# Optimization experiments

Measured on AMD Instinct MI355X. Metric: run time of the kernel, lower is better.

Reference implementation:

```python
import jax, jax.numpy as jnp
import numpy as np

N = 100000
E = 1600000
IN_CH = 128
HID = 32
HEADS = 8
OUT_CH = 40
NEG_SLOPE = 0.2


def _glorot(key, shape):
    fan = shape[0] + shape[-1]
    return jax.random.normal(key, shape, dtype=jnp.float32) * jnp.sqrt(2.0 / fan)


def gat_conv(x, src, dst, W, att_src, att_dst, bias, heads, out_ch, concat):
    # PyG GATConv (eval mode, dropout inactive, self-loops already appended)
    n = x.shape[0]
    h = (x @ W).reshape(n, heads, out_ch)              # [N,H,C]
    a_s = jnp.sum(h * att_src, axis=-1)                # [N,H]
    a_d = jnp.sum(h * att_dst, axis=-1)                # [N,H]
    e = jax.nn.leaky_relu(a_s[src] + a_d[dst], NEG_SLOPE)  # [E,H]
    # softmax over incoming edges of each destination node
    m = jax.ops.segment_max(e, dst, num_segments=n)
    e = jnp.exp(e - m[dst])
    denom = jax.ops.segment_sum(e, dst, num_segments=n)
    alpha = e / denom[dst]                              # [E,H]
    msg = h[src] * alpha[:, :, None]                    # [E,H,C] gather + weight
    out = jax.ops.segment_sum(msg, dst, num_segments=n)  # [N,H,C] scatter-add
    if concat:
        out = out.reshape(n, heads * out_ch)
    else:
        out = out.mean(axis=1)
    return out + bias


def setup_inputs() -> dict:
    key = jax.random.key(0)
    ks = jax.random.split(key, 16)
    x = jax.random.normal(ks[0], (N, IN_CH), dtype=jnp.float32)
    edge_index = jax.random.randint(ks[1], (2, E), 0, N, dtype=jnp.int64)
    params = {
        "W1": _glorot(ks[2], (IN_CH, HEADS * HID)),
        "as1": _glorot(ks[3], (HEADS, HID)),
        "ad1": _glorot(ks[4], (HEADS, HID)),
        "b1": jnp.zeros((HEADS * HID,), jnp.float32),
        "W2": _glorot(ks[5], (HEADS * HID, HID)),
        "as2": _glorot(ks[6], (1, HID)),
        "ad2": _glorot(ks[7], (1, HID)),
        "b2": jnp.zeros((HID,), jnp.float32),
        "W3": _glorot(ks[8], (HID, OUT_CH)),
        "as3": _glorot(ks[9], (1, OUT_CH)),
        "ad3": _glorot(ks[10], (1, OUT_CH)),
        "b3": jnp.zeros((OUT_CH,), jnp.float32),
    }
    return {"x": x, "edge_index": edge_index, **params}


def reference(x, edge_index, W1, as1, ad1, b1, W2, as2, ad2, b2, W3, as3, ad3, b3):
    n = x.shape[0]
    # PyG GATConv adds self-loops by default
    loops = jnp.arange(n, dtype=edge_index.dtype)
    src = jnp.concatenate([edge_index[0], loops])
    dst = jnp.concatenate([edge_index[1], loops])

    h = gat_conv(x, src, dst, W1, as1, ad1, b1, HEADS, HID, concat=True)
    h = jax.nn.elu(h)
    h = gat_conv(h, src, dst, W2, as2, ad2, b2, 1, HID, concat=False)
    h = jax.nn.elu(h)
    h = gat_conv(h, src, dst, W3, as3, ad3, b3, 1, OUT_CH, concat=False)
    return jax.nn.log_softmax(h, axis=1)
```

## Files before the change

kernel.cpp:

```cpp
#include <hip/hip_runtime.h>

#define NN 100000
#define NE 1600000
#define ET 1700000
#define NEG 0.2f
#define FNEG 3.4e38f
#define NBSC 98
#define GEMM1_NB 1563
#define PE_NB 6641
#define FATA_NB 8305

#define SRC_OFF   0ULL
#define DST_OFF   6800000ULL
#define RP_OFF    13600000ULL
#define CNT_OFF   14000128ULL
#define CSR_OFF   14400128ULL
#define W1F_OFF   21200128ULL
#define W2F_OFF   21265664ULL
#define W3F_OFF   21282048ULL
#define SC_OFF    21285120ULL
#define H_OFF     21286144ULL
#define H2B_OFF   72486144ULL
#define H3B_OFF   88486144ULL
#define ALPH_OFF  123686144ULL
#define ASN_OFF   150886144ULL
#define ADN_OFF   154086144ULL
#define AS2_OFF   157286144ULL
#define AD2_OFF   157686144ULL
#define WS_NEED   158086144ULL

typedef short bf16x8 __attribute__((ext_vector_type(8)));
typedef float f32x4 __attribute__((ext_vector_type(4)));

__device__ __forceinline__ float lrelu(float x) { return x > 0.f ? x : NEG * x; }
__device__ __forceinline__ float b2f(unsigned short u) {
  return __uint_as_float(((unsigned)u) << 16);
}
__device__ __forceinline__ unsigned short f2bu(float f) {
  unsigned u = __float_as_uint(f);
  return (unsigned short)((u + 0x7FFFu + ((u >> 16) & 1u)) >> 16);
}

__global__ __launch_bounds__(256) void k_sentinel(float* out, int n) {
  int i = blockIdx.x * 256 + threadIdx.x;
  if (i < n) out[i] = 12345.0f;
}

__global__ __launch_bounds__(256) void k_prep_w(const float* __restrict__ W1,
                                                const float* __restrict__ W2,
                                                const float* __restrict__ W3,
                                                unsigned short* __restrict__ W1f,
                                                unsigned short* __restrict__ W2f,
                                                unsigned short* __restrict__ W3f) {
  int idx = blockIdx.x * 256 + threadIdx.x;
  if (idx < 4096) {
    int fg = idx >> 6, lane = idx & 63;
    int mf = fg >> 2, kk = fg & 3;
    int c = mf * 16 + (lane & 15), k0 = kk * 32 + (lane >> 4) * 8;
    unsigned short* o = W1f + idx * 8;
    #pragma unroll
    for (int j = 0; j < 8; ++j) o[j] = f2bu(W1[(k0 + j) * 256 + c]);
  } else if (idx < 5120) {
    int t = idx - 4096;
    int fg = t >> 6, lane = t & 63;
    int mf = fg >> 3, kk = fg & 7;
    int c = mf * 16 + (lane & 15), k0 = kk * 32 + (lane >> 4) * 8;
    unsigned short* o = W2f + t * 8;
    #pragma unroll
    for (int j = 0; j < 8; ++j) o[j] = f2bu(W2[(k0 + j) * 32 + c]);
  } else if (idx < 5312) {
    int t = idx - 5120;
    int mf = t >> 6, lane = t & 63;
    int c = mf * 16 + (lane & 15), k0 = (lane >> 4) * 8;
    unsigned short* o = W3f + t * 8;
    #pragma unroll
    for (int j = 0; j < 8; ++j) o[j] = (c < 40) ? f2bu(W3[(k0 + j) * 40 + c]) : 0;
  }
}

__global__ __launch_bounds__(256) void k_fatA(const int* __restrict__ raw,
                                              int* __restrict__ src,
                                              int* __restrict__ dst,
                                              int* __restrict__ deg,
                                              const float* __restrict__ x,
                                              const bf16x8* __restrict__ W1f,
                                              const float* __restrict__ as1,
                                              const float* __restrict__ ad1,
                                              unsigned short* __restrict__ h,
                                              float* __restrict__ a_s,
                                              float* __restrict__ a_d) {
  __shared__ __align__(16) unsigned short xs[64 * 128];
  __shared__ float asL[256], adL[256];
  const int bid = blockIdx.x;
  const int grp = bid / 5, rem = bid - grp * 5;
  const int tid = threadIdx.x;

  if (rem != 4) {
    int pe = grp * 4 + rem;
    if (pe >= PE_NB) return;
    bool is64 = true;
    #pragma unroll
    for (int i = 1; i < 32; i += 2) is64 = is64 && (raw[i] == 0);
    long long e = (long long)pe * 256 + tid;
    if (e >= ET) return;
    int s, d;
    if (e < NE) {
      if (is64) {
        const long long* r = (const long long*)raw;
        s = (int)r[e];
        d = (int)r[NE + e];
      } else {
        s = raw[e];
        d = raw[NE + e];
      }
    } else {
      s = d = (int)(e - NE);
    }
    src[e] = s;
    dst[e] = d;
    atomicAdd(&deg[d], 1);
    return;
  }

  if (grp >= GEMM1_NB) return;
  const int n0 = grp * 64;
  asL[tid] = as1[tid];
  adL[tid] = ad1[tid];
  for (int j = tid; j < 2048; j += 256) {
    int r = j >> 5;
    int c4 = (j & 31) << 2;
    long long row = n0 + r; if (row >= NN) row = NN - 1;
    float4 v = *(const float4*)(x + row * 128 + c4);
    unsigned short* p = &xs[r * 128 + c4];
    p[0] = f2bu(v.x); p[1] = f2bu(v.y); p[2] = f2bu(v.z); p[3] = f2bu(v.w);
  }
  __syncthreads();
  const int w = tid >> 6, lane = tid & 63;
  const int nloc = w * 16 + (lane & 15);
  const int node = n0 + nloc;
  bf16x8 bfr[4];
  #pragma unroll
  for (int kk = 0; kk < 4; ++kk)
    bfr[kk] = *(const bf16x8*)&xs[nloc * 128 + kk * 32 + (lane >> 4) * 8];
  const int ch_base = (lane >> 4) * 4;
  float sA[8] = {}, sD[8] = {};
  #pragma unroll
  for (int mf = 0; mf < 16; ++mf) {
    f32x4 acc = {0.f, 0.f, 0.f, 0.f};
    #pragma unroll
    for (int kk = 0; kk < 4; ++kk) {
      bf16x8 af = W1f[(mf * 4 + kk) * 64 + lane];
      acc = __builtin_amdgcn_mfma_f32_16x16x32_bf16(af, bfr[kk], acc, 0, 0, 0);
    }
    const float* av = &asL[mf * 16 + ch_base];
    const float* dv = &adL[mf * 16 + ch_base];
    float ps = acc[0] * av[0] + acc[1] * av[1] + acc[2] * av[2] + acc[3] * av[3];
    float pd = acc[0] * dv[0] + acc[1] * dv[1] + acc[2] * dv[2] + acc[3] * dv[3];
    ps += __shfl_xor(ps, 16); ps += __shfl_xor(ps, 32);
    pd += __shfl_xor(pd, 16); pd += __shfl_xor(pd, 32);
    sA[mf >> 1] += ps; sD[mf >> 1] += pd;
    if (node < NN) {
      ushort4 o;
      o.x = f2bu(acc[0]); o.y = f2bu(acc[1]); o.z = f2bu(acc[2]); o.w = f2bu(acc[3]);
      *(ushort4*)&h[(unsigned)(node * 256 + mf * 16 + ch_base)] = o;
    }
  }
  if (lane < 16 && node < NN) {
    #pragma unroll
    for (int hd = 0; hd < 8; ++hd) {
      a_s[node * 8 + hd] = sA[hd];
      a_d[node * 8 + hd] = sD[hd];
    }
  }
}

__global__ __launch_bounds__(1024) void k_scan_a(const int* __restrict__ deg,
                                                 int* __restrict__ rowptr,
                                                 int* __restrict__ bsum) {
  __shared__ int wsum[16];
  const int lane = threadIdx.x & 63, wid = threadIdx.x >> 6;
  int i = blockIdx.x * 1024 + threadIdx.x;
  int x = (i < NN) ? deg[i] : 0;
  int inc = x;
  #pragma unroll
  for (int off = 1; off < 64; off <<= 1) {
    int t = __shfl_up(inc, off);
    if (lane >= off) inc += t;
  }
  if (lane == 63) wsum[wid] = inc;
  __syncthreads();
  if (wid == 0) {
    int w = (lane < 16) ? wsum[lane] : 0;
    #pragma unroll
    for (int off = 1; off < 16; off <<= 1) {
      int t = __shfl_up(w, off);
      if (lane >= off) w += t;
    }
    if (lane < 16) wsum[lane] = w;
  }
  __syncthreads();
  int base = wid ? wsum[wid - 1] : 0;
  if (i < NN) rowptr[i + 1] = base + inc;
  if (threadIdx.x == 1023) bsum[blockIdx.x] = base + inc;
}

__global__ __launch_bounds__(128) void k_scan_b(int* __restrict__ bsum) {
  __shared__ int w0tot;
  int tid = threadIdx.x;
  int v = (tid < NBSC) ? bsum[tid] : 0;
  int inc = v;
  #pragma unroll
  for (int off = 1; off < 64; off <<= 1) {
    int t = __shfl_up(inc, off);
    if ((tid & 63) >= off) inc += t;
  }
  if (tid == 63) w0tot = inc;
  __syncthreads();
  if (tid >= 64) inc += w0tot;
  if (tid < NBSC) bsum[tid] = inc - v;
}

__global__ __launch_bounds__(1024) void k_scan_c(int* __restrict__ rowptr,
                                                 const int* __restrict__ bsum,
                                                 int* __restrict__ cnt) {
  int i = blockIdx.x * 1024 + threadIdx.x;
  if (i < NN) {
    rowptr[i + 1] += bsum[blockIdx.x];
    cnt[i] = 0;
  }
  if (i == 0) rowptr[0] = 0;
}

__global__ __launch_bounds__(256) void k_fill(const int* __restrict__ src,
                                              const int* __restrict__ dst,
                                              const int* __restrict__ rowptr,
                                              int* __restrict__ cnt,
                                              int* __restrict__ csr) {
  long long e = (long long)blockIdx.x * 256 + threadIdx.x;
  if (e >= ET) return;
  int d = dst[e];
  int p = atomicAdd(&cnt[d], 1);
  csr[rowptr[d] + p] = src[e];
}

__global__ __launch_bounds__(256) void k_msalpha1(const int* __restrict__ rowptr,
                                                  const int* __restrict__ csr,
                                                  const float* __restrict__ a_s,
                                                  const float* __restrict__ a_d,
                                                  unsigned short* __restrict__ alph) {
  const int node = blockIdx.x * 4 + (threadIdx.x >> 6);
  const int lane = threadIdx.x & 63;
  const int beg = __builtin_amdgcn_readfirstlane(rowptr[node]);
  const int end = __builtin_amdgcn_readfirstlane(rowptr[node + 1]);
  const int hd = lane & 7;
  const int eg = lane >> 3;
  const float adv = a_d[node * 8 + hd];
  float mx = -FNEG, sm = 0.f;
  if (end - beg <= 32) {
    float vc0 = 0.f, vc1 = 0.f, vc2 = 0.f, vc3 = 0.f;
    #pragma unroll
    for (int k = 0; k < 4; ++k) {
      int i = beg + eg + k * 8;
      if (i < end) {
        float v = lrelu(a_s[csr[i] * 8 + hd] + adv);
        if (k == 0) vc0 = v; else if (k == 1) vc1 = v;
        else if (k == 2) vc2 = v; else vc3 = v;
        float nm = fmaxf(mx, v);
        sm = sm * __expf(mx - nm) + __expf(v - nm);
        mx = nm;
      }
    }
    #pragma unroll
    for (int off = 8; off < 64; off <<= 1) {
      float mo = __shfl_xor(mx, off);
      float so = __shfl_xor(sm, off);
      float nm = fmaxf(mx, mo);
      sm = sm * __expf(mx - nm) + so * __expf(mo - nm);
      mx = nm;
    }
    float rden = 1.0f / sm;
    #pragma unroll
    for (int k = 0; k < 4; ++k) {
      int i = beg + eg + k * 8;
      if (i < end) {
        float v = (k == 0) ? vc0 : (k == 1) ? vc1 : (k == 2) ? vc2 : vc3;
        alph[i * 8 + hd] = f2bu(__expf(v - mx) * rden);
      }
    }
  } else {
    for (int i = beg + eg; i < end; i += 8) {
      int s = csr[i];
      float v = lrelu(a_s[s * 8 + hd] + adv);
      float nm = fmaxf(mx, v);
      sm = sm * __expf(mx - nm) + __expf(v - nm);
      mx = nm;
    }
    #pragma unroll
    for (int off = 8; off < 64; off <<= 1) {
      float mo = __shfl_xor(mx, off);
      float so = __shfl_xor(sm, off);
      float nm = fmaxf(mx, mo);
      sm = sm * __expf(mx - nm) + so * __expf(mo - nm);
      mx = nm;
    }
    float rden = 1.0f / sm;
    for (int i = beg + eg; i < end; i += 8) {
      int s = csr[i];
      float v = lrelu(a_s[s * 8 + hd] + adv);
      alph[i * 8 + hd] = f2bu(__expf(v - mx) * rden);
    }
  }
}

__global__ __launch_bounds__(1024) void k_gather1f(const int* __restrict__ rowptr,
                                                   const int* __restrict__ csr,
                                                   const unsigned short* __restrict__ alph,
                                                   const unsigned short* __restrict__ h,
                                                   const float* __restrict__ b,
                                                   const bf16x8* __restrict__ W2f,
                                                   const float* __restrict__ as2,
                                                   const float* __restrict__ ad2,
                                                   unsigned short* __restrict__ h2,
                                                   float* __restrict__ a_s,
                                                   float* __restrict__ a_d) {
  __shared__ __align__(16) unsigned short xs[16 * 256];
  const int tid = threadIdx.x;
  const int w = tid >> 6, lane = tid & 63;
  const int n0 = blockIdx.x * 16;
  const int node = n0 + w;
  const int beg = __builtin_amdgcn_readfirstlane(rowptr[node]);
  const int end = __builtin_amdgcn_readfirstlane(rowptr[node + 1]);
  const int hd2 = lane >> 3;
  const unsigned l4 = lane * 4;
  float4 acc = {0.f, 0.f, 0.f, 0.f};
  int i = beg;
  for (; i + 8 <= end; i += 8) {
    int s0 = __builtin_amdgcn_readfirstlane(csr[i]);
    int s1 = __builtin_amdgcn_readfirstlane(csr[i + 1]);
    int s2 = __builtin_amdgcn_readfirstlane(csr[i + 2]);
    int s3 = __builtin_amdgcn_readfirstlane(csr[i + 3]);
    int s4 = __builtin_amdgcn_readfirstlane(csr[i + 4]);
    int s5 = __builtin_amdgcn_readfirstlane(csr[i + 5]);
    int s6 = __builtin_amdgcn_readfirstlane(csr[i + 6]);
    int s7 = __builtin_amdgcn_readfirstlane(csr[i + 7]);
    float a0 = b2f(alph[(i + 0) * 8 + hd2]);
    float a1 = b2f(alph[(i + 1) * 8 + hd2]);
    float a2 = b2f(alph[(i + 2) * 8 + hd2]);
    float a3 = b2f(alph[(i + 3) * 8 + hd2]);
    float a4 = b2f(alph[(i + 4) * 8 + hd2]);
    float a5 = b2f(alph[(i + 5) * 8 + hd2]);
    float a6 = b2f(alph[(i + 6) * 8 + hd2]);
    float a7 = b2f(alph[(i + 7) * 8 + hd2]);
    ushort4 h0 = *(const ushort4*)(h + ((unsigned)(s0 << 8) + l4));
    ushort4 h1 = *(const ushort4*)(h + ((unsigned)(s1 << 8) + l4));
    ushort4 h2v = *(const ushort4*)(h + ((unsigned)(s2 << 8) + l4));
    ushort4 h3v = *(const ushort4*)(h + ((unsigned)(s3 << 8) + l4));
    ushort4 h4v = *(const ushort4*)(h + ((unsigned)(s4 << 8) + l4));
    ushort4 h5v = *(const ushort4*)(h + ((unsigned)(s5 << 8) + l4));
    ushort4 h6v = *(const ushort4*)(h + ((unsigned)(s6 << 8) + l4));
    ushort4 h7v = *(const ushort4*)(h + ((unsigned)(s7 << 8) + l4));
    acc.x += a0 * b2f(h0.x) + a1 * b2f(h1.x) + a2 * b2f(h2v.x) + a3 * b2f(h3v.x)
           + a4 * b2f(h4v.x) + a5 * b2f(h5v.x) + a6 * b2f(h6v.x) + a7 * b2f(h7v.x);
    acc.y += a0 * b2f(h0.y) + a1 * b2f(h1.y) + a2 * b2f(h2v.y) + a3 * b2f(h3v.y)
           + a4 * b2f(h4v.y) + a5 * b2f(h5v.y) + a6 * b2f(h6v.y) + a7 * b2f(h7v.y);
    acc.z += a0 * b2f(h0.z) + a1 * b2f(h1.z) + a2 * b2f(h2v.z) + a3 * b2f(h3v.z)
           + a4 * b2f(h4v.z) + a5 * b2f(h5v.z) + a6 * b2f(h6v.z) + a7 * b2f(h7v.z);
    acc.w += a0 * b2f(h0.w) + a1 * b2f(h1.w) + a2 * b2f(h2v.w) + a3 * b2f(h3v.w)
           + a4 * b2f(h4v.w) + a5 * b2f(h5v.w) + a6 * b2f(h6v.w) + a7 * b2f(h7v.w);
  }
  for (; i + 4 <= end; i += 4) {
    int s0 = __builtin_amdgcn_readfirstlane(csr[i]);
    int s1 = __builtin_amdgcn_readfirstlane(csr[i + 1]);
    int s2 = __builtin_amdgcn_readfirstlane(csr[i + 2]);
    int s3 = __builtin_amdgcn_readfirstlane(csr[i + 3]);
    float a0 = b2f(alph[(i + 0) * 8 + hd2]);
    float a1 = b2f(alph[(i + 1) * 8 + hd2]);
    float a2 = b2f(alph[(i + 2) * 8 + hd2]);
    float a3 = b2f(alph[(i + 3) * 8 + hd2]);
    ushort4 h0 = *(const ushort4*)(h + ((unsigned)(s0 << 8) + l4));
    ushort4 h1 = *(const ushort4*)(h + ((unsigned)(s1 << 8) + l4));
    ushort4 h2v = *(const ushort4*)(h + ((unsigned)(s2 << 8) + l4));
    ushort4 h3v = *(const ushort4*)(h + ((unsigned)(s3 << 8) + l4));
    acc.x += a0 * b2f(h0.x) + a1 * b2f(h1.x) + a2 * b2f(h2v.x) + a3 * b2f(h3v.x);
    acc.y += a0 * b2f(h0.y) + a1 * b2f(h1.y) + a2 * b2f(h2v.y) + a3 * b2f(h3v.y);
    acc.z += a0 * b2f(h0.z) + a1 * b2f(h1.z) + a2 * b2f(h2v.z) + a3 * b2f(h3v.z);
    acc.w += a0 * b2f(h0.w) + a1 * b2f(h1.w) + a2 * b2f(h2v.w) + a3 * b2f(h3v.w);
  }
  for (; i < end; ++i) {
    int s0 = __builtin_amdgcn_readfirstlane(csr[i]);
    float a0 = b2f(alph[i * 8 + hd2]);
    ushort4 h0 = *(const ushort4*)(h + ((unsigned)(s0 << 8) + l4));
    acc.x += a0 * b2f(h0.x);
    acc.y += a0 * b2f(h0.y);
    acc.z += a0 * b2f(h0.z);
    acc.w += a0 * b2f(h0.w);
  }
  float4 bv = *(const float4*)(b + l4);
  acc.x += bv.x; acc.y += bv.y; acc.z += bv.z; acc.w += bv.w;
  acc.x = acc.x > 0.f ? acc.x : expm1f(acc.x);
  acc.y = acc.y > 0.f ? acc.y : expm1f(acc.y);
  acc.z = acc.z > 0.f ? acc.z : expm1f(acc.z);
  acc.w = acc.w > 0.f ? acc.w : expm1f(acc.w);
  {
    ushort4 o;
    o.x = f2bu(acc.x); o.y = f2bu(acc.y); o.z = f2bu(acc.z); o.w = f2bu(acc.w);
    *(ushort4*)&xs[w * 256 + l4] = o;
  }
  __syncthreads();
  if (w == 0) {
    const int nloc = lane & 15;
    const int node2 = n0 + nloc;
    const int ch_base = (lane >> 4) * 4;
    float sA = 0.f, sD = 0.f;
    #pragma unroll
    for (int mf = 0; mf < 2; ++mf) {
      f32x4 c2 = {0.f, 0.f, 0.f, 0.f};
      #pragma unroll
      for (int kk = 0; kk < 8; ++kk) {
        bf16x8 bfr = *(const bf16x8*)&xs[nloc * 256 + kk * 32 + (lane >> 4) * 8];
        c2 = __builtin_amdgcn_mfma_f32_16x16x32_bf16(W2f[(mf * 8 + kk) * 64 + lane],
                                                     bfr, c2, 0, 0, 0);
      }
      float4 av = *(const float4*)(as2 + mf * 16 + ch_base);
      float4 dv = *(const float4*)(ad2 + mf * 16 + ch_base);
      float ps = c2[0] * av.x + c2[1] * av.y + c2[2] * av.z + c2[3] * av.w;
      float pd = c2[0] * dv.x + c2[1] * dv.y + c2[2] * dv.z + c2[3] * dv.w;
      ps += __shfl_xor(ps, 16); ps += __shfl_xor(ps, 32);
      pd += __shfl_xor(pd, 16); pd += __shfl_xor(pd, 32);
      sA += ps; sD += pd;
      ushort4 o;
      o.x = f2bu(c2[0]); o.y = f2bu(c2[1]); o.z = f2bu(c2[2]); o.w = f2bu(c2[3]);
      *(ushort4*)&h2[(unsigned)(node2 * 32 + mf * 16 + ch_base)] = o;
    }
    if (lane < 16) { a_s[node2] = sA; a_d[node2] = sD; }
  }
}

__global__ __launch_bounds__(512) void k_gather2f(const int* __restrict__ rowptr,
                                                  const int* __restrict__ csr,
                                                  const float* __restrict__ a_s,
                                                  const float* __restrict__ a_d,
                                                  const unsigned short* __restrict__ h,
                                                  const float* __restrict__ b,
                                                  const bf16x8* __restrict__ W3f,
                                                  const float* __restrict__ as3,
                                                  const float* __restrict__ ad3,
                                                  unsigned short* __restrict__ h3,
                                                  float* __restrict__ a_s3,
                                                  float* __restrict__ a_d3) {
  __shared__ __align__(16) unsigned short xs[16 * 32];
  const int tid = threadIdx.x;
  const int hw = tid >> 5, lane32 = tid & 31;
  const int n0 = blockIdx.x * 16;
  const int node = n0 + hw;
  const int beg = rowptr[node], end = rowptr[node + 1];
  const float adv = a_d[node];

  float mx = -FNEG, sm = 0.f;
  for (int i = beg + lane32; i < end; i += 32) {
    float v = lrelu(a_s[csr[i]] + adv);
    float nm = fmaxf(mx, v);
    sm = sm * __expf(mx - nm) + __expf(v - nm);
    mx = nm;
  }
  #pragma unroll
  for (int off = 1; off < 32; off <<= 1) {
    float mo = __shfl_xor(mx, off, 32);
    float so = __shfl_xor(sm, off, 32);
    float nm = fmaxf(mx, mo);
    sm = sm * __expf(mx - nm) + so * __expf(mo - nm);
    mx = nm;
  }
  float rden = 1.0f / sm;

  float acc = 0.f;
  int i = beg;
  for (; i + 4 <= end; i += 4) {
    int s0 = csr[i], s1 = csr[i + 1], s2 = csr[i + 2], s3 = csr[i + 3];
    float a0 = __expf(lrelu(a_s[s0] + adv) - mx) * rden;
    float a1 = __expf(lrelu(a_s[s1] + adv) - mx) * rden;
    float a2 = __expf(lrelu(a_s[s2] + adv) - mx) * rden;
    float a3 = __expf(lrelu(a_s[s3] + adv) - mx) * rden;
    unsigned short v0 = h[(unsigned)(s0 * 32 + lane32)];
    unsigned short v1 = h[(unsigned)(s1 * 32 + lane32)];
    unsigned short v2 = h[(unsigned)(s2 * 32 + lane32)];
    unsigned short v3 = h[(unsigned)(s3 * 32 + lane32)];
    acc += a0 * b2f(v0) + a1 * b2f(v1) + a2 * b2f(v2) + a3 * b2f(v3);
  }
  for (; i < end; ++i) {
    int s0 = csr[i];
    float a0 = __expf(lrelu(a_s[s0] + adv) - mx) * rden;
    acc += a0 * b2f(h[(unsigned)(s0 * 32 + lane32)]);
  }
  acc += b[lane32];
  acc = acc > 0.f ? acc : expm1f(acc);
  xs[hw * 32 + lane32] = f2bu(acc);
  __syncthreads();
  if (tid < 64) {
    const int lane = tid;
    const int nloc = lane & 15;
    const int node3 = n0 + nloc;
    const int ch_base = (lane >> 4) * 4;
    bf16x8 bfr = *(const bf16x8*)&xs[nloc * 32 + (lane >> 4) * 8];
    float sA = 0.f, sD = 0.f;
    #pragma unroll
    for (int mf = 0; mf < 3; ++mf) {
      f32x4 c3 = {0.f, 0.f, 0.f, 0.f};
      c3 = __builtin_amdgcn_mfma_f32_16x16x32_bf16(W3f[mf * 64 + lane], bfr, c3, 0, 0, 0);
      int ch0 = mf * 16 + ch_base;
      float4 av = {0.f, 0.f, 0.f, 0.f}, dv = {0.f, 0.f, 0.f, 0.f};
      if (ch0 < 40) {
        av = *(const float4*)(as3 + ch0);
        dv = *(const float4*)(ad3 + ch0);
      }
      float ps = c3[0] * av.x + c3[1] * av.y + c3[2] * av.z + c3[3] * av.w;
      float pd = c3[0] * dv.x + c3[1] * dv.y + c3[2] * dv.z + c3[3] * dv.w;
      ps += __shfl_xor(ps, 16); ps += __shfl_xor(ps, 32);
      pd += __shfl_xor(pd, 16); pd += __shfl_xor(pd, 32);
      sA += ps; sD += pd;
      if (ch0 < 40) {
        ushort4 o;
        o.x = f2bu(c3[0]); o.y = f2bu(c3[1]); o.z = f2bu(c3[2]); o.w = f2bu(c3[3]);
        *(ushort4*)&h3[(unsigned)(node3 * 40 + ch0)] = o;
      }
    }
    if (lane < 16) { a_s3[node3] = sA; a_d3[node3] = sD; }
  }
}

__global__ __launch_bounds__(256) void k_gather3f(const int* __restrict__ rowptr,
                                                  const int* __restrict__ csr,
                                                  const float* __restrict__ a_s,
                                                  const float* __restrict__ a_d,
                                                  const unsigned short* __restrict__ h,
                                                  const float* __restrict__ b,
                                                  float* __restrict__ out) {
  const int node = blockIdx.x * 4 + (threadIdx.x >> 6);
  const int lane = threadIdx.x & 63;
  const int beg = __builtin_amdgcn_readfirstlane(rowptr[node]);
  const int end = __builtin_amdgcn_readfirstlane(rowptr[node + 1]);
  const float adv = a_d[node];

  float mx = -FNEG, sm = 0.f;
  for (int i = beg + lane; i < end; i += 64) {
    float v = lrelu(a_s[csr[i]] + adv);
    float nm = fmaxf(mx, v);
    sm = sm * __expf(mx - nm) + __expf(v - nm);
    mx = nm;
  }
  #pragma unroll
  for (int off = 1; off < 64; off <<= 1) {
    float mo = __shfl_xor(mx, off);
    float so = __shfl_xor(sm, off);
    float nm = fmaxf(mx, mo);
    sm = sm * __expf(mx - nm) + so * __expf(mo - nm);
    mx = nm;
  }
  float rden = 1.0f / sm;

  float acc = 0.f;
  int i = beg;
  for (; i + 4 <= end; i += 4) {
    int s0 = __builtin_amdgcn_readfirstlane(csr[i]);
    int s1 = __builtin_amdgcn_readfirstlane(csr[i + 1]);
    int s2 = __builtin_amdgcn_readfirstlane(csr[i + 2]);
    int s3 = __builtin_amdgcn_readfirstlane(csr[i + 3]);
    float a0 = __expf(lrelu(a_s[s0] + adv) - mx) * rden;
    float a1 = __expf(lrelu(a_s[s1] + adv) - mx) * rden;
    float a2 = __expf(lrelu(a_s[s2] + adv) - mx) * rden;
    float a3 = __expf(lrelu(a_s[s3] + adv) - mx) * rden;
    if (lane < 40) {
      unsigned short v0 = h[(unsigned)(s0 * 40 + lane)];
      unsigned short v1 = h[(unsigned)(s1 * 40 + lane)];
      unsigned short v2 = h[(unsigned)(s2 * 40 + lane)];
      unsigned short v3 = h[(unsigned)(s3 * 40 + lane)];
      acc += a0 * b2f(v0) + a1 * b2f(v1) + a2 * b2f(v2) + a3 * b2f(v3);
    }
  }
  for (; i < end; ++i) {
    int s0 = __builtin_amdgcn_readfirstlane(csr[i]);
    float a0 = __expf(lrelu(a_s[s0] + adv) - mx) * rden;
    if (lane < 40) acc += a0 * b2f(h[(unsigned)(s0 * 40 + lane)]);
  }
  float v = (lane < 40) ? acc + b[lane] : -FNEG;
  float vmax = v;
  #pragma unroll
  for (int off = 1; off < 64; off <<= 1) vmax = fmaxf(vmax, __shfl_xor(vmax, off));
  float ex = (lane < 40) ? __expf(v - vmax) : 0.f;
  float es = ex;
  #pragma unroll
  for (int off = 1; off < 64; off <<= 1) es += __shfl_xor(es, off);
  float lse = vmax + __logf(es);
  if (lane < 40) out[(long long)node * 40 + lane] = v - lse;
}

extern "C" void kernel_launch(void* const* d_in, const int* in_sizes, int n_in,
                              void* d_out, int out_size, void* d_ws, size_t ws_size,
                              hipStream_t stream) {
  const float* x   = (const float*)d_in[0];
  const int*   eix = (const int*)d_in[1];
  const float* W1  = (const float*)d_in[2];
  const float* as1 = (const float*)d_in[3];
  const float* ad1 = (const float*)d_in[4];
  const float* b1  = (const float*)d_in[5];
  const float* W2  = (const float*)d_in[6];
  const float* as2 = (const float*)d_in[7];
  const float* ad2 = (const float*)d_in[8];
  const float* b2  = (const float*)d_in[9];
  const float* W3  = (const float*)d_in[10];
  const float* as3 = (const float*)d_in[11];
  const float* ad3 = (const float*)d_in[12];
  const float* b3  = (const float*)d_in[13];
  float* out = (float*)d_out;

  if (ws_size < WS_NEED) {
    k_sentinel<<<(out_size + 255) / 256, 256, 0, stream>>>(out, out_size);
    return;
  }

  char* ws = (char*)d_ws;
  int*    src    = (int*)(ws + SRC_OFF);
  int*    dst    = (int*)(ws + DST_OFF);
  int*    rowptr = (int*)(ws + RP_OFF);
  int*    cnt    = (int*)(ws + CNT_OFF);
  int*    csr    = (int*)(ws + CSR_OFF);
  unsigned short* W1f = (unsigned short*)(ws + W1F_OFF);
  unsigned short* W2f = (unsigned short*)(ws + W2F_OFF);
  unsigned short* W3f = (unsigned short*)(ws + W3F_OFF);
  int*    bsum   = (int*)(ws + SC_OFF);
  unsigned short* h1b  = (unsigned short*)(ws + H_OFF);
  unsigned short* h2b  = (unsigned short*)(ws + H2B_OFF);
  unsigned short* h3b  = (unsigned short*)(ws + H3B_OFF);
  unsigned short* alph = (unsigned short*)(ws + ALPH_OFF);
  float*  aS     = (float*)(ws + ASN_OFF);
  float*  aD     = (float*)(ws + ADN_OFF);
  float*  aS2    = (float*)(ws + AS2_OFF);
  float*  aD2    = (float*)(ws + AD2_OFF);

  hipMemsetAsync(ws + CNT_OFF, 0, 400000, stream);
  k_prep_w<<<21, 256, 0, stream>>>(W1, W2, W3, W1f, W2f, W3f);
  k_fatA<<<FATA_NB, 256, 0, stream>>>(eix, src, dst, cnt, x, (const bf16x8*)W1f,
                                      as1, ad1, h1b, aS, aD);
  k_scan_a<<<NBSC, 1024, 0, stream>>>(cnt, rowptr, bsum);
  k_scan_b<<<1, 128, 0, stream>>>(bsum);
  k_scan_c<<<NBSC, 1024, 0, stream>>>(rowptr, bsum, cnt);
  k_fill<<<(ET + 255) / 256, 256, 0, stream>>>(src, dst, rowptr, cnt, csr);

  k_msalpha1<<<NN / 4, 256, 0, stream>>>(rowptr, csr, aS, aD, alph);
  k_gather1f<<<NN / 16, 1024, 0, stream>>>(rowptr, csr, alph, h1b, b1,
                                           (const bf16x8*)W2f, as2, ad2,
                                           h2b, aS, aD);

  k_gather2f<<<NN / 16, 512, 0, stream>>>(rowptr, csr, aS, aD, h2b, b2,
                                          (const bf16x8*)W3f, as3, ad3,
                                          h3b, aS2, aD2);

  k_gather3f<<<NN / 4, 256, 0, stream>>>(rowptr, csr, aS2, aD2, h3b, b3, out);
}
```

Baseline: 474.6 us.

## Record atomic ranks with striped degree counters to make CSR fill atomic-free

Degree counting now uses 8 striped counter arrays, selected by edge index mod 8, and stores each edge's atomic return value as its rank. The scan turns the striped counts into per-stripe offsets, so the CSR fill kernel can place each edge without atomics and handles four edges per thread. This removes the second atomic pass and reduces counter contention. In exchange it costs a larger memset, an extra rank array write and read, and strided counter reads in the scan.

Result: faster. 434.5 us (-8.4%).

```diff
diff --git a/kernel.cpp b/kernel.cpp
--- a/kernel.cpp
+++ b/kernel.cpp
@@ -9,11 +9,11 @@
 #define GEMM1_NB 1563
 #define PE_NB 6641
 #define FATA_NB 8305
+#define FILL_CH 425000
 
 #define SRC_OFF   0ULL
 #define DST_OFF   6800000ULL
 #define RP_OFF    13600000ULL
-#define CNT_OFF   14000128ULL
 #define CSR_OFF   14400128ULL
 #define W1F_OFF   21200128ULL
 #define W2F_OFF   21265664ULL
@@ -27,7 +27,9 @@
 #define ADN_OFF   154086144ULL
 #define AS2_OFF   157286144ULL
 #define AD2_OFF   157686144ULL
-#define WS_NEED   158086144ULL
+#define CNT8_OFF  158086144ULL
+#define RANK_OFF  161286144ULL
+#define WS_NEED   168086144ULL
 
 typedef short bf16x8 __attribute__((ext_vector_type(8)));
 typedef float f32x4 __attribute__((ext_vector_type(4)));
@@ -81,7 +83,8 @@
 __global__ __launch_bounds__(256) void k_fatA(const int* __restrict__ raw,
                                               int* __restrict__ src,
                                               int* __restrict__ dst,
-                                              int* __restrict__ deg,
+                                              int* __restrict__ cnt8,
+                                              int* __restrict__ rank,
                                               const float* __restrict__ x,
                                               const bf16x8* __restrict__ W1f,
                                               const float* __restrict__ as1,
@@ -118,7 +121,7 @@
     }
     src[e] = s;
     dst[e] = d;
-    atomicAdd(&deg[d], 1);
+    rank[e] = atomicAdd(&cnt8[(tid & 7) * NN + d], 1);
     return;
   }
 
@@ -174,13 +177,23 @@
   }
 }
 
-__global__ __launch_bounds__(1024) void k_scan_a(const int* __restrict__ deg,
+__global__ __launch_bounds__(1024) void k_scan_a(int* __restrict__ cnt8,
                                                  int* __restrict__ rowptr,
                                                  int* __restrict__ bsum) {
   __shared__ int wsum[16];
   const int lane = threadIdx.x & 63, wid = threadIdx.x >> 6;
   int i = blockIdx.x * 1024 + threadIdx.x;
-  int x = (i < NN) ? deg[i] : 0;
+  int x = 0;
+  if (i < NN) {
+    int run = 0;
+    #pragma unroll
+    for (int k = 0; k < 8; ++k) {
+      int c = cnt8[k * NN + i];
+      cnt8[k * NN + i] = run;
+      run += c;
+    }
+    x = run;
+  }
   int inc = x;
   #pragma unroll
   for (int off = 1; off < 64; off <<= 1) {
@@ -221,26 +234,32 @@
 }
 
 __global__ __launch_bounds__(1024) void k_scan_c(int* __restrict__ rowptr,
-                                                 const int* __restrict__ bsum,
-                                                 int* __restrict__ cnt) {
+                                                 const int* __restrict__ bsum) {
   int i = blockIdx.x * 1024 + threadIdx.x;
-  if (i < NN) {
-    rowptr[i + 1] += bsum[blockIdx.x];
-    cnt[i] = 0;
-  }
+  if (i < NN) rowptr[i + 1] += bsum[blockIdx.x];
   if (i == 0) rowptr[0] = 0;
 }
 
-__global__ __launch_bounds__(256) void k_fill(const int* __restrict__ src,
-                                              const int* __restrict__ dst,
-                                              const int* __restrict__ rowptr,
-                                              int* __restrict__ cnt,
-                                              int* __restrict__ csr) {
-  long long e = (long long)blockIdx.x * 256 + threadIdx.x;
-  if (e >= ET) return;
-  int d = dst[e];
-  int p = atomicAdd(&cnt[d], 1);
-  csr[rowptr[d] + p] = src[e];
+__global__ __launch_bounds__(256) void k_fill_nr(const int* __restrict__ src,
+                                                 const int* __restrict__ dst,
+                                                 const int* __restrict__ rank,
+                                                 const int* __restrict__ cnt8,
+                                                 const int* __restrict__ rowptr,
+                                                 int* __restrict__ csr) {
+  int gid = blockIdx.x * 256 + threadIdx.x;
+  if (gid >= FILL_CH) return;
+  const int h = gid & 7;
+  int e0 = gid, e1 = gid + FILL_CH, e2 = gid + 2 * FILL_CH, e3 = gid + 3 * FILL_CH;
+  int d0 = dst[e0], d1 = dst[e1], d2 = dst[e2], d3 = dst[e3];
+  int r0 = rank[e0], r1 = rank[e1], r2 = rank[e2], r3 = rank[e3];
+  int s0 = src[e0], s1 = src[e1], s2 = src[e2], s3 = src[e3];
+  int p0 = cnt8[h * NN + d0], p1 = cnt8[h * NN + d1];
+  int p2 = cnt8[h * NN + d2], p3 = cnt8[h * NN + d3];
+  int b0 = rowptr[d0], b1 = rowptr[d1], b2 = rowptr[d2], b3 = rowptr[d3];
+  csr[b0 + p0 + r0] = s0;
+  csr[b1 + p1 + r1] = s1;
+  csr[b2 + p2 + r2] = s2;
+  csr[b3 + p3 + r3] = s3;
 }
 
 __global__ __launch_bounds__(256) void k_msalpha1(const int* __restrict__ rowptr,
@@ -622,7 +641,6 @@
   int*    src    = (int*)(ws + SRC_OFF);
   int*    dst    = (int*)(ws + DST_OFF);
   int*    rowptr = (int*)(ws + RP_OFF);
-  int*    cnt    = (int*)(ws + CNT_OFF);
   int*    csr    = (int*)(ws + CSR_OFF);
   unsigned short* W1f = (unsigned short*)(ws + W1F_OFF);
   unsigned short* W2f = (unsigned short*)(ws + W2F_OFF);
@@ -636,15 +654,18 @@
   float*  aD     = (float*)(ws + ADN_OFF);
   float*  aS2    = (float*)(ws + AS2_OFF);
   float*  aD2    = (float*)(ws + AD2_OFF);
-
-  hipMemsetAsync(ws + CNT_OFF, 0, 400000, stream);
+  int*    cnt8   = (int*)(ws + CNT8_OFF);
+  int*    rank   = (int*)(ws + RANK_OFF);
+
+  hipMemsetAsync(ws + CNT8_OFF, 0, 3200000, stream);
   k_prep_w<<<21, 256, 0, stream>>>(W1, W2, W3, W1f, W2f, W3f);
-  k_fatA<<<FATA_NB, 256, 0, stream>>>(eix, src, dst, cnt, x, (const bf16x8*)W1f,
-                                      as1, ad1, h1b, aS, aD);
-  k_scan_a<<<NBSC, 1024, 0, stream>>>(cnt, rowptr, bsum);
+  k_fatA<<<FATA_NB, 256, 0, stream>>>(eix, src, dst, cnt8, rank, x,
+                                      (const bf16x8*)W1f, as1, ad1, h1b, aS, aD);
+  k_scan_a<<<NBSC, 1024, 0, stream>>>(cnt8, rowptr, bsum);
   k_scan_b<<<1, 128, 0, stream>>>(bsum);
-  k_scan_c<<<NBSC, 1024, 0, stream>>>(rowptr, bsum, cnt);
-  k_fill<<<(ET + 255) / 256, 256, 0, stream>>>(src, dst, rowptr, cnt, csr);
+  k_scan_c<<<NBSC, 1024, 0, stream>>>(rowptr, bsum);
+  k_fill_nr<<<(FILL_CH + 255) / 256, 256, 0, stream>>>(src, dst, rank, cnt8,
+                                                       rowptr, csr);
 
   k_msalpha1<<<NN / 4, 256, 0, stream>>>(rowptr, csr, aS, aD, alph);
   k_gather1f<<<NN / 16, 1024, 0, stream>>>(rowptr, csr, alph, h1b, b1,
```
